# Kernel optimization log

Hardware: AMD Instinct MI355X
Metric: run time of the kernel (lower is better)

## Reference

```python
import jax, jax.numpy as jnp
import numpy as np
import math

B, S, E, H = 2, 2048, 1024, 16
D = E // H  # head dim = 64


def setup_inputs() -> dict:
    key = jax.random.key(0)
    ks = jax.random.split(key, 7)
    scale = 1.0 / math.sqrt(E)
    return {
        "query": jax.random.normal(ks[0], (B, S, E), dtype=jnp.float32),
        "key": jax.random.normal(ks[1], (B, S, E), dtype=jnp.float32),
        "value": jax.random.normal(ks[2], (B, S, E), dtype=jnp.float32),
        # packed in-projection: (3E, E) weights, (3E,) bias, q/k/v order
        "in_proj_weight": jax.random.normal(ks[3], (3 * E, E), dtype=jnp.float32) * scale,
        "in_proj_bias": jnp.zeros((3 * E,), dtype=jnp.float32),
        "out_proj_weight": jax.random.normal(ks[4], (E, E), dtype=jnp.float32) * scale,
        "out_proj_bias": jnp.zeros((E,), dtype=jnp.float32),
    }


def reference(query, key, value, in_proj_weight, in_proj_bias, out_proj_weight, out_proj_bias):
    # packed in-projection (q, k, v order), F.linear convention: x @ W^T + b
    w_q, w_k, w_v = jnp.split(in_proj_weight, 3, axis=0)
    b_q, b_k, b_v = jnp.split(in_proj_bias, 3, axis=0)
    q = query @ w_q.T + b_q   # [B, S, E]
    k = key @ w_k.T + b_k
    v = value @ w_v.T + b_v

    # split heads: [B, S, E] -> [B, H, S, D]
    def heads(x):
        return x.reshape(B, S, H, D).transpose(0, 2, 1, 3)

    q, k, v = heads(q), heads(k), heads(v)
    q = q / jnp.asarray(math.sqrt(D), dtype=q.dtype)

    # naive softmax attention (materializes [B, H, S, S] as original bmm+softmax+bmm)
    scores = jnp.einsum("bhqd,bhkd->bhqk", q, k)
    attn = jax.nn.softmax(scores, axis=-1)
    out = jnp.einsum("bhqk,bhkd->bhqd", attn, v)  # [B, H, S, D]

    out = out.transpose(0, 2, 1, 3).reshape(B, S, E)
    return out @ out_proj_weight.T + out_proj_bias
```

## Files before the change

### kernel.cpp

```cpp
#include <hip/hip_runtime.h>
#include <stdint.h>

#define LOG2E 1.44269504088896340736f

typedef __bf16 bf16x8 __attribute__((ext_vector_type(8)));
typedef float f32x4 __attribute__((ext_vector_type(4)));
typedef float f32x16 __attribute__((ext_vector_type(16)));

static constexpr int Bb = 2, Ss = 2048, Ee = 1024, Hh = 16, Dd = 64;
static constexpr int BSE = Bb * Ss * Ee;

static constexpr size_t OFF_QB    = 0;
static constexpr size_t OFF_KB    = 4194304;
static constexpr size_t OFF_VB    = 8388608;
static constexpr size_t OFF_WQKV  = 12582912;
static constexpr size_t OFF_WOUT  = 15728640;
static constexpr size_t OFF_QH    = 16777216;
static constexpr size_t OFF_KH    = 20971520;
static constexpr size_t OFF_VH    = 25165824;
static constexpr size_t OFF_OB    = 29360128;

__device__ __forceinline__ uint16_t f32_bf16(float f) {
    uint32_t u = __builtin_bit_cast(uint32_t, f);
    u += 0x7fffu + ((u >> 16) & 1u);
    return (uint16_t)(u >> 16);
}

__device__ __forceinline__ uint32_t cvt_pk_bf16(float a, float b) {
    uint32_t r;
    asm("v_cvt_pk_bf16_f32 %0, %1, %2" : "=v"(r) : "v"(a), "v"(b));
    return r;
}

__device__ __forceinline__ void perm32swap(uint32_t& x, uint32_t& y) {
    asm("v_permlane32_swap_b32 %0, %1" : "+v"(x), "+v"(y));
}

__global__ __launch_bounds__(256) void cvt_kernel(
    const float* __restrict__ q, const float* __restrict__ k, const float* __restrict__ v,
    const float* __restrict__ w1, const float* __restrict__ w2, uint16_t* __restrict__ ws)
{
    const float* srcs[5] = {q, k, v, w1, w2};
    const int ns4[5] = {BSE/4, BSE/4, BSE/4, (3*Ee*Ee)/4, (Ee*Ee)/4};
    uint16_t* dsts[5] = {ws+OFF_QB, ws+OFF_KB, ws+OFF_VB, ws+OFF_WQKV, ws+OFF_WOUT};
    int z = blockIdx.z;
    int i = blockIdx.x * blockDim.x + threadIdx.x;
    if (i < ns4[z]) {
        float4 f = ((const float4*)srcs[z])[i];
        ushort4 o;
        o.x = f32_bf16(f.x); o.y = f32_bf16(f.y);
        o.z = f32_bf16(f.z); o.w = f32_bf16(f.w);
        ((ushort4*)dsts[z])[i] = o;
    }
}

template<int MODE>
__global__ __launch_bounds__(256) void gemm_nt(
    const uint16_t* __restrict__ Aq, const uint16_t* __restrict__ Ak,
    const uint16_t* __restrict__ Av, const uint16_t* __restrict__ Bw,
    const float* __restrict__ bias, uint16_t* __restrict__ OutB,
    float* __restrict__ OutF)
{
    constexpr int K = Ee, N = Ee;
    const int tid = threadIdx.x;
    const int l = tid & 63, w = tid >> 6;
    const int wr = w >> 1, wc = w & 1;
    const int tm = blockIdx.y, tn = blockIdx.x;
    const int z = (MODE == 0) ? blockIdx.z : 0;

    const uint16_t* A = (MODE == 0) ? (z == 0 ? Aq : (z == 1 ? Ak : Av)) : Aq;
    const uint16_t* Bp = Bw + (size_t)z * Ee * Ee;
    const float* bp = bias + (size_t)z * Ee;

    __shared__ alignas(16) uint16_t As[128 * 32];
    __shared__ alignas(16) uint16_t Bs[128 * 32];

    f32x4 acc[4][4] = {};
    const int arow = tm * 128;
    const int bcol = tn * 128;

    for (int kt = 0; kt < K / 32; ++kt) {
        __syncthreads();
        #pragma unroll
        for (int it = 0; it < 2; ++it) {
            int c = tid + it * 256;
            int row = c >> 2, qq = c & 3;
            const uint16_t* ga = A  + (size_t)(arow + row) * K + kt * 32 + qq * 8;
            const uint16_t* gb = Bp + (size_t)(bcol + row) * K + kt * 32 + qq * 8;
            __builtin_amdgcn_global_load_lds(
                (const __attribute__((address_space(1))) void*)ga,
                (__attribute__((address_space(3))) void*)(As + c * 8), 16, 0, 0);
            __builtin_amdgcn_global_load_lds(
                (const __attribute__((address_space(1))) void*)gb,
                (__attribute__((address_space(3))) void*)(Bs + c * 8), 16, 0, 0);
        }
        __syncthreads();
        bf16x8 aF[4], bF[4];
        #pragma unroll
        for (int m = 0; m < 4; ++m)
            aF[m] = *(const bf16x8*)(As + ((wr * 64 + m * 16 + (l & 15)) * 32 + (l >> 4) * 8));
        #pragma unroll
        for (int n = 0; n < 4; ++n)
            bF[n] = *(const bf16x8*)(Bs + ((wc * 64 + n * 16 + (l & 15)) * 32 + (l >> 4) * 8));
        #pragma unroll
        for (int m = 0; m < 4; ++m)
            #pragma unroll
            for (int n = 0; n < 4; ++n)
                acc[m][n] = __builtin_amdgcn_mfma_f32_16x16x32_bf16(aF[m], bF[n], acc[m][n], 0, 0, 0);
    }

    #pragma unroll
    for (int n = 0; n < 4; ++n) {
        int col = bcol + wc * 64 + n * 16 + (l & 15);
        float bn = bp[col];
        #pragma unroll
        for (int m = 0; m < 4; ++m) {
            int row0 = arow + wr * 64 + m * 16 + (l >> 4) * 4;
            #pragma unroll
            for (int j = 0; j < 4; ++j) {
                int row = row0 + j;
                float v = acc[m][n][j] + bn;
                if (MODE == 0) {
                    if (z == 0) v *= 0.125f;
                    int b = row >> 11, s = row & 2047, hh = col >> 6, d = col & 63;
                    OutB[(size_t)z * BSE + (size_t)(((b * Hh) + hh) * Ss + s) * Dd + d] = f32_bf16(v);
                } else {
                    OutF[(size_t)row * N + col] = v;
                }
            }
        }
    }
}

__global__ __launch_bounds__(256, 2) void attn_kernel(
    const uint16_t* __restrict__ Qh, const uint16_t* __restrict__ Kh,
    const uint16_t* __restrict__ Vh, uint16_t* __restrict__ O)
{
    const int tid = threadIdx.x;
    const int l = tid & 63, w = tid >> 6;
    const int q = l & 31, hi = l >> 5;
    const int bh = blockIdx.y;
    const int q0 = blockIdx.x * 128;
    const size_t base = (size_t)bh * Ss * Dd;

    __shared__ alignas(16) uint16_t Vt[64 * 64];

    bf16x8 qf[4];
    {
        const uint16_t* qp = Qh + base + (size_t)(q0 + w * 32 + q) * Dd + hi * 8;
        #pragma unroll
        for (int m = 0; m < 4; ++m) qf[m] = *(const bf16x8*)(qp + 16 * m);
    }

    const int kp = tid >> 3, c8 = tid & 7;
    uint4 kreg[8];
    uint4 vr0, vr1;

    auto loadK = [&](int key0) {
        const uint16_t* kpp = Kh + base + (size_t)(key0 + q) * Dd + hi * 8;
        #pragma unroll
        for (int t2 = 0; t2 < 2; ++t2)
            #pragma unroll
            for (int m = 0; m < 4; ++m)
                kreg[t2 * 4 + m] = *(const uint4*)(kpp + (size_t)t2 * 32 * Dd + 16 * m);
    };
    auto loadV = [&](int key0) {
        const uint16_t* vp = Vh + base + (size_t)(key0 + 2 * kp) * Dd + c8 * 8;
        vr0 = *(const uint4*)vp;
        vr1 = *(const uint4*)(vp + Dd);
    };

    loadK(0);
    loadV(0);

    f32x16 o0 = {}, o1 = {};
    float lsum = 0.f;

    auto build_pb = [&](const f32x16& sv, bf16x8* pbout) {
        float p[16];
        #pragma unroll
        for (int r2 = 0; r2 < 16; ++r2) {
            p[r2] = __builtin_amdgcn_exp2f(sv[r2] * LOG2E - 8.0f * LOG2E);
            lsum += p[r2];
        }
        uint32_t W[4][2];
        #pragma unroll
        for (int a = 0; a < 4; ++a) {
            W[a][0] = cvt_pk_bf16(p[4 * a + 0], p[4 * a + 1]);
            W[a][1] = cvt_pk_bf16(p[4 * a + 2], p[4 * a + 3]);
        }
        #pragma unroll
        for (int kl = 0; kl < 2; ++kl) {
            uint32_t x0 = W[2 * kl][0], x1 = W[2 * kl][1];
            uint32_t y0 = W[2 * kl + 1][0], y1 = W[2 * kl + 1][1];
            perm32swap(x0, y0);
            perm32swap(x1, y1);
            union { uint32_t u[4]; bf16x8 v; } pu;
            pu.u[0] = x0; pu.u[1] = x1; pu.u[2] = y0; pu.u[3] = y1;
            pbout[kl] = pu.v;
        }
    };

    for (int kt = 0; kt < Ss / 64; ++kt) {
        __syncthreads();
        {
            const uint16_t* e0 = (const uint16_t*)&vr0;
            const uint16_t* e1 = (const uint16_t*)&vr1;
            #pragma unroll
            for (int e = 0; e < 8; ++e) {
                int d = c8 * 8 + e;
                int swz = (kp >> 2) ^ e ^ c8;
                uint32_t pk = (uint32_t)e0[e] | ((uint32_t)e1[e] << 16);
                *(uint32_t*)&Vt[d * 64 + swz * 8 + ((2 * kp) & 7)] = pk;
            }
        }
        __syncthreads();

        f32x16 s0 = {}, s1 = {};
        __builtin_amdgcn_s_setprio(1);
        #pragma unroll
        for (int m = 0; m < 4; ++m)
            s0 = __builtin_amdgcn_mfma_f32_32x32x16_bf16(
                __builtin_bit_cast(bf16x8, kreg[m]), qf[m], s0, 0, 0, 0);
        #pragma unroll
        for (int m = 0; m < 4; ++m)
            s1 = __builtin_amdgcn_mfma_f32_32x32x16_bf16(
                __builtin_bit_cast(bf16x8, kreg[4 + m]), qf[m], s1, 0, 0, 0);
        __builtin_amdgcn_s_setprio(0);

        if (kt < Ss / 64 - 1) {
            loadK((kt + 1) * 64);
            loadV((kt + 1) * 64);
        }

        bf16x8 pb[4];
        build_pb(s0, pb + 0);
        build_pb(s1, pb + 2);

        __builtin_amdgcn_s_setprio(1);
        #pragma unroll
        for (int ka = 0; ka < 4; ++ka) {
            #pragma unroll
            for (int dt = 0; dt < 2; ++dt) {
                int d = 32 * dt + q;
                int swz = (2 * ka + hi) ^ (d & 7) ^ (d >> 3);
                bf16x8 vf = *(const bf16x8*)&Vt[d * 64 + swz * 8];
                if (dt == 0)
                    o0 = __builtin_amdgcn_mfma_f32_32x32x16_bf16(vf, pb[ka], o0, 0, 0, 0);
                else
                    o1 = __builtin_amdgcn_mfma_f32_32x32x16_bf16(vf, pb[ka], o1, 0, 0, 0);
            }
        }
        __builtin_amdgcn_s_setprio(0);
    }

    float lr = lsum + __shfl_xor(lsum, 32);
    float inv = 1.0f / lr;

    const int bq = bh >> 4, hh = bh & 15;
    const int srow = q0 + w * 32 + q;
    uint16_t* orow = O + (size_t)(bq * Ss + srow) * Ee + hh * Dd;
    #pragma unroll
    for (int dt = 0; dt < 2; ++dt) {
        const f32x16& oo = dt ? o1 : o0;
        #pragma unroll
        for (int rg = 0; rg < 4; ++rg) {
            int d0 = 32 * dt + 8 * rg + 4 * hi;
            uint32_t w0 = cvt_pk_bf16(oo[4 * rg + 0] * inv, oo[4 * rg + 1] * inv);
            uint32_t w1 = cvt_pk_bf16(oo[4 * rg + 2] * inv, oo[4 * rg + 3] * inv);
            uint2 pk; pk.x = w0; pk.y = w1;
            *(uint2*)&orow[d0] = pk;
        }
    }
}

extern "C" void kernel_launch(void* const* d_in, const int* in_sizes, int n_in,
                              void* d_out, int out_size, void* d_ws, size_t ws_size,
                              hipStream_t stream) {
    (void)in_sizes; (void)n_in; (void)out_size; (void)ws_size;
    const float* query = (const float*)d_in[0];
    const float* key   = (const float*)d_in[1];
    const float* value = (const float*)d_in[2];
    const float* w_in  = (const float*)d_in[3];
    const float* b_in  = (const float*)d_in[4];
    const float* w_out = (const float*)d_in[5];
    const float* b_out = (const float*)d_in[6];
    uint16_t* ws = (uint16_t*)d_ws;

    uint16_t* qb    = ws + OFF_QB;
    uint16_t* kb    = ws + OFF_KB;
    uint16_t* vb    = ws + OFF_VB;
    uint16_t* wqkvb = ws + OFF_WQKV;
    uint16_t* woutb = ws + OFF_WOUT;
    uint16_t* Qh    = ws + OFF_QH;
    uint16_t* Kh    = ws + OFF_KH;
    uint16_t* Vh    = ws + OFF_VH;
    uint16_t* Ob    = ws + OFF_OB;

    cvt_kernel<<<dim3(4096, 1, 5), 256, 0, stream>>>(query, key, value, w_in, w_out, ws);
    gemm_nt<0><<<dim3(8, 32, 3), 256, 0, stream>>>(qb, kb, vb, wqkvb, b_in, Qh, nullptr);
    attn_kernel<<<dim3(Ss / 128, Bb * Hh), 256, 0, stream>>>(Qh, Kh, Vh, Ob);
    gemm_nt<1><<<dim3(8, 32, 1), 256, 0, stream>>>(Ob, nullptr, nullptr, woutb, b_out, nullptr, (float*)d_out);
}
```

Baseline: 148.3 us.

## Split attention over key halves with fp32 partials and combine kernel

Attention now splits the key range into two halves, so the grid doubles to 1024 blocks. Blocks are remapped in XCD-aware order, and K is staged through double-buffered swizzled LDS alongside V. Partial unnormalized outputs and row sums go to fp32 scratch buffers, and a new combine kernel sums them and normalizes. The out-proj weight conversion is moved after attention because the partials reuse the workspace region. This aims to raise occupancy and parallelism, at the cost of extra global traffic for the fp32 partials and two extra launches.

```diff
diff --git a/kernel.cpp b/kernel.cpp
--- a/kernel.cpp
+++ b/kernel.cpp
@@ -38,11 +38,11 @@
 
 __global__ __launch_bounds__(256) void cvt_kernel(
     const float* __restrict__ q, const float* __restrict__ k, const float* __restrict__ v,
-    const float* __restrict__ w1, const float* __restrict__ w2, uint16_t* __restrict__ ws)
-{
-    const float* srcs[5] = {q, k, v, w1, w2};
-    const int ns4[5] = {BSE/4, BSE/4, BSE/4, (3*Ee*Ee)/4, (Ee*Ee)/4};
-    uint16_t* dsts[5] = {ws+OFF_QB, ws+OFF_KB, ws+OFF_VB, ws+OFF_WQKV, ws+OFF_WOUT};
+    const float* __restrict__ w1, uint16_t* __restrict__ ws)
+{
+    const float* srcs[4] = {q, k, v, w1};
+    const int ns4[4] = {BSE/4, BSE/4, BSE/4, (3*Ee*Ee)/4};
+    uint16_t* dsts[4] = {ws+OFF_QB, ws+OFF_KB, ws+OFF_VB, ws+OFF_WQKV};
     int z = blockIdx.z;
     int i = blockIdx.x * blockDim.x + threadIdx.x;
     if (i < ns4[z]) {
@@ -52,6 +52,17 @@
         o.z = f32_bf16(f.z); o.w = f32_bf16(f.w);
         ((ushort4*)dsts[z])[i] = o;
     }
+}
+
+__global__ __launch_bounds__(256) void cvt_one(
+    const float* __restrict__ src, uint16_t* __restrict__ dst)
+{
+    int i = blockIdx.x * 256 + threadIdx.x;
+    float4 f = ((const float4*)src)[i];
+    ushort4 o;
+    o.x = f32_bf16(f.x); o.y = f32_bf16(f.y);
+    o.z = f32_bf16(f.z); o.w = f32_bf16(f.w);
+    ((ushort4*)dst)[i] = o;
 }
 
 template<int MODE>
@@ -132,18 +143,25 @@
     }
 }
 
-__global__ __launch_bounds__(256, 2) void attn_kernel(
+__global__ __launch_bounds__(256, 4) void attn_kernel(
     const uint16_t* __restrict__ Qh, const uint16_t* __restrict__ Kh,
-    const uint16_t* __restrict__ Vh, uint16_t* __restrict__ O)
+    const uint16_t* __restrict__ Vh, float* __restrict__ po,
+    float* __restrict__ lpart)
 {
     const int tid = threadIdx.x;
     const int l = tid & 63, w = tid >> 6;
     const int q = l & 31, hi = l >> 5;
-    const int bh = blockIdx.y;
-    const int q0 = blockIdx.x * 128;
+
+    const int orig = blockIdx.x;
+    const int L = (orig & 7) * 128 + (orig >> 3);
+    const int qb = L & 15, split = (L >> 4) & 1, bh = L >> 5;
+
+    const int q0 = qb * 128;
+    const int keyb = split * 1024;
     const size_t base = (size_t)bh * Ss * Dd;
 
-    __shared__ alignas(16) uint16_t Vt[64 * 64];
+    __shared__ alignas(16) uint16_t Ks[2][64 * 64];
+    __shared__ alignas(16) uint16_t Vt[2][64 * 64];
 
     bf16x8 qf[4];
     {
@@ -152,26 +170,20 @@
         for (int m = 0; m < 4; ++m) qf[m] = *(const bf16x8*)(qp + 16 * m);
     }
 
-    const int kp = tid >> 3, c8 = tid & 7;
-    uint4 kreg[8];
-    uint4 vr0, vr1;
-
-    auto loadK = [&](int key0) {
-        const uint16_t* kpp = Kh + base + (size_t)(key0 + q) * Dd + hi * 8;
-        #pragma unroll
-        for (int t2 = 0; t2 < 2; ++t2)
-            #pragma unroll
-            for (int m = 0; m < 4; ++m)
-                kreg[t2 * 4 + m] = *(const uint4*)(kpp + (size_t)t2 * 32 * Dd + 16 * m);
+    const int kp = tid >> 3, c8v = tid & 7;
+    uint4 kg[2], vg0, vg1;
+
+    auto loadKV = [&](int key0) {
+        #pragma unroll
+        for (int it = 0; it < 2; ++it) {
+            int c = tid + 256 * it;
+            kg[it] = *(const uint4*)(Kh + base + (size_t)(key0 + (c >> 3)) * Dd + (c & 7) * 8);
+        }
+        vg0 = *(const uint4*)(Vh + base + (size_t)(key0 + 2 * kp) * Dd + c8v * 8);
+        vg1 = *(const uint4*)(Vh + base + (size_t)(key0 + 2 * kp + 1) * Dd + c8v * 8);
     };
-    auto loadV = [&](int key0) {
-        const uint16_t* vp = Vh + base + (size_t)(key0 + 2 * kp) * Dd + c8 * 8;
-        vr0 = *(const uint4*)vp;
-        vr1 = *(const uint4*)(vp + Dd);
-    };
-
-    loadK(0);
-    loadV(0);
+
+    loadKV(keyb);
 
     f32x16 o0 = {}, o1 = {};
     float lsum = 0.f;
@@ -201,37 +213,42 @@
         }
     };
 
-    for (int kt = 0; kt < Ss / 64; ++kt) {
+    for (int kt = 0; kt < 16; ++kt) {
+        const int b = kt & 1;
         __syncthreads();
+
         {
-            const uint16_t* e0 = (const uint16_t*)&vr0;
-            const uint16_t* e1 = (const uint16_t*)&vr1;
+            #pragma unroll
+            for (int it = 0; it < 2; ++it) {
+                int c = tid + 256 * it, row = c >> 3, cc = c & 7;
+                *(uint4*)&Ks[b][row * 64 + ((cc ^ (row & 7)) << 3)] = kg[it];
+            }
+            const uint16_t* e0 = (const uint16_t*)&vg0;
+            const uint16_t* e1 = (const uint16_t*)&vg1;
             #pragma unroll
             for (int e = 0; e < 8; ++e) {
-                int d = c8 * 8 + e;
-                int swz = (kp >> 2) ^ e ^ c8;
-                uint32_t pk = (uint32_t)e0[e] | ((uint32_t)e1[e] << 16);
-                *(uint32_t*)&Vt[d * 64 + swz * 8 + ((2 * kp) & 7)] = pk;
+                int d = c8v * 8 + e;
+                int swz = (kp >> 2) ^ e ^ c8v;
+                uint32_t pk2 = (uint32_t)e0[e] | ((uint32_t)e1[e] << 16);
+                *(uint32_t*)&Vt[b][d * 64 + swz * 8 + ((2 * kp) & 7)] = pk2;
             }
         }
+
+        if (kt < 15) loadKV(keyb + (kt + 1) * 64);
+
         __syncthreads();
 
         f32x16 s0 = {}, s1 = {};
         __builtin_amdgcn_s_setprio(1);
         #pragma unroll
-        for (int m = 0; m < 4; ++m)
-            s0 = __builtin_amdgcn_mfma_f32_32x32x16_bf16(
-                __builtin_bit_cast(bf16x8, kreg[m]), qf[m], s0, 0, 0, 0);
-        #pragma unroll
-        for (int m = 0; m < 4; ++m)
-            s1 = __builtin_amdgcn_mfma_f32_32x32x16_bf16(
-                __builtin_bit_cast(bf16x8, kreg[4 + m]), qf[m], s1, 0, 0, 0);
+        for (int m = 0; m < 4; ++m) {
+            int sw = ((2 * m + hi) ^ (q & 7)) << 3;
+            bf16x8 k0 = *(const bf16x8*)&Ks[b][q * 64 + sw];
+            bf16x8 k1 = *(const bf16x8*)&Ks[b][(32 + q) * 64 + sw];
+            s0 = __builtin_amdgcn_mfma_f32_32x32x16_bf16(k0, qf[m], s0, 0, 0, 0);
+            s1 = __builtin_amdgcn_mfma_f32_32x32x16_bf16(k1, qf[m], s1, 0, 0, 0);
+        }
         __builtin_amdgcn_s_setprio(0);
-
-        if (kt < Ss / 64 - 1) {
-            loadK((kt + 1) * 64);
-            loadV((kt + 1) * 64);
-        }
 
         bf16x8 pb[4];
         build_pb(s0, pb + 0);
@@ -244,7 +261,7 @@
             for (int dt = 0; dt < 2; ++dt) {
                 int d = 32 * dt + q;
                 int swz = (2 * ka + hi) ^ (d & 7) ^ (d >> 3);
-                bf16x8 vf = *(const bf16x8*)&Vt[d * 64 + swz * 8];
+                bf16x8 vf = *(const bf16x8*)&Vt[b][d * 64 + swz * 8];
                 if (dt == 0)
                     o0 = __builtin_amdgcn_mfma_f32_32x32x16_bf16(vf, pb[ka], o0, 0, 0, 0);
                 else
@@ -255,23 +272,38 @@
     }
 
     float lr = lsum + __shfl_xor(lsum, 32);
-    float inv = 1.0f / lr;
-
-    const int bq = bh >> 4, hh = bh & 15;
-    const int srow = q0 + w * 32 + q;
-    uint16_t* orow = O + (size_t)(bq * Ss + srow) * Ee + hh * Dd;
+    const int qrow = q0 + w * 32 + q;
+    const size_t rowbase = ((size_t)(split * 32 + bh) * 2048 + qrow) * 64;
     #pragma unroll
     for (int dt = 0; dt < 2; ++dt) {
         const f32x16& oo = dt ? o1 : o0;
         #pragma unroll
-        for (int rg = 0; rg < 4; ++rg) {
-            int d0 = 32 * dt + 8 * rg + 4 * hi;
-            uint32_t w0 = cvt_pk_bf16(oo[4 * rg + 0] * inv, oo[4 * rg + 1] * inv);
-            uint32_t w1 = cvt_pk_bf16(oo[4 * rg + 2] * inv, oo[4 * rg + 3] * inv);
-            uint2 pk; pk.x = w0; pk.y = w1;
-            *(uint2*)&orow[d0] = pk;
-        }
-    }
+        for (int a = 0; a < 4; ++a) {
+            float4 st;
+            st.x = oo[4 * a + 0]; st.y = oo[4 * a + 1];
+            st.z = oo[4 * a + 2]; st.w = oo[4 * a + 3];
+            *(float4*)&po[rowbase + 32 * dt + 8 * a + 4 * hi] = st;
+        }
+    }
+    if (hi == 0)
+        lpart[(size_t)(split * 32 + bh) * 2048 + qrow] = lr;
+}
+
+__global__ __launch_bounds__(256) void combine_kernel(
+    const float* __restrict__ po, const float* __restrict__ lp,
+    uint16_t* __restrict__ Ob)
+{
+    int gi = blockIdx.x * 256 + threadIdx.x;
+    int row = gi >> 4, c4 = gi & 15;
+    float4 a  = *(const float4*)&po[(size_t)row * 64 + c4 * 4];
+    float4 b2 = *(const float4*)&po[4194304 + (size_t)row * 64 + c4 * 4];
+    float inv = 1.0f / (lp[row] + lp[65536 + row]);
+    int bh = row >> 11, qrow = row & 2047;
+    int bb = bh >> 4, hh = bh & 15;
+    ushort4 o;
+    o.x = f32_bf16((a.x + b2.x) * inv); o.y = f32_bf16((a.y + b2.y) * inv);
+    o.z = f32_bf16((a.z + b2.z) * inv); o.w = f32_bf16((a.w + b2.w) * inv);
+    *(ushort4*)&Ob[(size_t)(bb * 2048 + qrow) * 1024 + hh * 64 + c4 * 4] = o;
 }
 
 extern "C" void kernel_launch(void* const* d_in, const int* in_sizes, int n_in,
@@ -296,9 +328,13 @@
     uint16_t* Kh    = ws + OFF_KH;
     uint16_t* Vh    = ws + OFF_VH;
     uint16_t* Ob    = ws + OFF_OB;
-
-    cvt_kernel<<<dim3(4096, 1, 5), 256, 0, stream>>>(query, key, value, w_in, w_out, ws);
+    float*    po    = (float*)d_ws;
+    float*    lpart = (float*)d_out;
+
+    cvt_kernel<<<dim3(4096, 1, 4), 256, 0, stream>>>(query, key, value, w_in, ws);
     gemm_nt<0><<<dim3(8, 32, 3), 256, 0, stream>>>(qb, kb, vb, wqkvb, b_in, Qh, nullptr);
-    attn_kernel<<<dim3(Ss / 128, Bb * Hh), 256, 0, stream>>>(Qh, Kh, Vh, Ob);
+    attn_kernel<<<dim3(1024), 256, 0, stream>>>(Qh, Kh, Vh, po, lpart);
+    combine_kernel<<<dim3(4096), 256, 0, stream>>>(po, lpart, Ob);
+    cvt_one<<<dim3(1024), 256, 0, stream>>>(w_out, woutb);
     gemm_nt<1><<<dim3(8, 32, 1), 256, 0, stream>>>(Ob, nullptr, nullptr, woutb, b_out, nullptr, (float*)d_out);
 }
```

New measurement: 212.6 us. +43.4%, slower.
